# Kernel optimization log

Hardware: AMD Instinct MI355X
Metric: run time of the kernel (lower is better)

The kernel has to match this reference:

```python
import jax, jax.numpy as jnp
import numpy as np
import math

D = 128
SAMPLE_RATE = 16000
F_MIN = 40.0
WINDOW_SAMPLES = 400
DECAY_C = 4.0
B, L = 8, 80000


def _mel_freqs(num, f_min, f_max):
    m_min = 2595.0 * np.log10(1.0 + f_min / 700.0)
    m_max = 2595.0 * np.log10(1.0 + f_max / 700.0)
    mels = np.linspace(m_min, m_max, num)
    return 700.0 * (10.0 ** (mels / 2595.0) - 1.0)


def setup_inputs() -> dict:
    key = jax.random.key(0)
    k_x, k_phase = jax.random.split(key)
    x = jax.random.normal(k_x, (B, L), dtype=jnp.float32)

    freqs_hz = _mel_freqs(D, F_MIN, SAMPLE_RATE / 2)
    omega = jnp.asarray(2.0 * math.pi * freqs_hz / SAMPLE_RATE, dtype=jnp.float32)

    alpha_mag = DECAY_C / WINDOW_SAMPLES  # 0.01
    alpha_raw = jnp.full((D,), math.log(math.expm1(alpha_mag)), dtype=jnp.float32)
    b_log_mag = jnp.full((D,), math.log(math.sqrt(2.0 * alpha_mag)), dtype=jnp.float32)
    b_phase = 2.0 * math.pi * jax.random.uniform(k_phase, (D,), dtype=jnp.float32)

    # K = ceil(log(1/1e-5)/alpha_mag) rounded up to 64, clipped to [64, L] -> 1152
    K = int(math.ceil(math.log(1.0 / 1e-5) / alpha_mag))
    K = max(64, min(K, L))
    K = (K + 63) // 64 * 64
    K = min(K, L)

    return {"x": x, "omega": omega, "alpha_raw": alpha_raw,
            "b_log_mag": b_log_mag, "b_phase": b_phase, "K": K}


def reference(x, omega, alpha_raw, b_log_mag, b_phase, K):
    # Analytic Gabor taps: g(tau) = |b| * exp(alpha*tau) * exp(i*(phi + omega*tau))
    alpha = -jax.nn.softplus(alpha_raw)            # (D,), alpha < 0
    b_mag = jnp.exp(b_log_mag)                     # (D,)
    tau = jnp.arange(K, dtype=x.dtype)             # (K,)
    envelope = jnp.exp(alpha[None, :] * tau[:, None])          # (K, D)
    phase = b_phase[None, :] + omega[None, :] * tau[:, None]   # (K, D)
    scale = b_mag[None, :] * envelope
    g_real = scale * jnp.cos(phase)                # (K, D)
    g_imag = scale * jnp.sin(phase)                # (K, D)

    # Causal correlation with flipped taps -> causal FIR convolution.
    # weight: (2D, 1, K) = [real filters; imag filters]
    g_real_f = jnp.flip(g_real, axis=0).T          # (D, K)
    g_imag_f = jnp.flip(g_imag, axis=0).T          # (D, K)
    weight = jnp.concatenate([g_real_f, g_imag_f], axis=0)[:, None, :]  # (2D,1,K)

    x_padded = jnp.pad(x[:, None, :], ((0, 0), (0, 0), (K - 1, 0)))  # (B,1,L+K-1)
    H = jax.lax.conv_general_dilated(
        x_padded, weight, window_strides=(1,), padding='VALID',
        dimension_numbers=('NCW', 'OIW', 'NCW'))   # (B, 2D, L)

    H_real, H_imag = H[:, :D, :], H[:, D:, :]
    power = H_real * H_real + H_imag * H_imag      # |H|^2, return_power=True path
    return jnp.transpose(power, (0, 2, 1))         # (B, L, D)
```

## Files before the change

### kernel.cpp

```cpp
#include <hip/hip_runtime.h>
#include <math.h>


#define BB 8
#define LL 80000
#define DD 128
#define CHUNK 500
#define NCHUNK 160
#define KMAX 1152

#define STEP(xv)                                   \
    {                                              \
        float t1 = fmaf(-ei, si, (xv));            \
        float nr = fmaf(er, sr, t1);               \
        float ni = fmaf(er, si, ei * sr);          \
        sr = nr; si = ni;                          \
    }

__global__ __launch_bounds__(DD) void sstfr_kernel(
    const float* __restrict__ x,
    const float* __restrict__ omega,
    const float* __restrict__ alpha_raw,
    const float* __restrict__ b_log_mag,
    const int*   __restrict__ Kp,
    float*       __restrict__ out)
{
    __shared__ __align__(16) float xs[KMAX + CHUNK];

    const int d     = threadIdx.x;
    const int chunk = blockIdx.x;
    const int b     = blockIdx.y;

    int K = Kp[0];
    K = (K + 3) & ~3;
    if (K > KMAX) K = KMAX;

    const int t0    = chunk * CHUNK;
    const int base  = t0 - K;
    const int total = CHUNK + K;
    const float* xb = x + (size_t)b * LL;

    for (int i = d; i < total; i += DD) {
        const int idx = base + i;
        xs[i] = (idx >= 0 && idx < LL) ? xb[idx] : 0.0f;
    }
    __syncthreads();

    const float w     = omega[d];
    const float alpha = -log1pf(expf(alpha_raw[d]));
    const float ea    = expf(alpha);
    const float er    = ea * cosf(w);
    const float ei    = ea * sinf(w);
    const float scale = expf(2.0f * b_log_mag[d]);

    float sr = 0.0f, si = 0.0f;

    const float4* x4 = (const float4*)xs;
    const int g0 = K >> 2;
    const int gT = total >> 2;

    float4 cur = x4[0];

    for (int q = 0; q < g0; ++q) {
        float4 nxt = x4[q + 1];
        STEP(cur.x) STEP(cur.y) STEP(cur.z) STEP(cur.w)
        cur = nxt;
    }

    float* op = out + ((size_t)b * LL + t0) * DD + d;
    for (int q = g0; q < gT - 1; ++q) {
        float4 nxt = x4[q + 1];
        STEP(cur.x) op[0 * DD] = scale * fmaf(sr, sr, si * si);
        STEP(cur.y) op[1 * DD] = scale * fmaf(sr, sr, si * si);
        STEP(cur.z) op[2 * DD] = scale * fmaf(sr, sr, si * si);
        STEP(cur.w) op[3 * DD] = scale * fmaf(sr, sr, si * si);
        op += 4 * DD;
        cur = nxt;
    }
    STEP(cur.x) op[0 * DD] = scale * fmaf(sr, sr, si * si);
    STEP(cur.y) op[1 * DD] = scale * fmaf(sr, sr, si * si);
    STEP(cur.z) op[2 * DD] = scale * fmaf(sr, sr, si * si);
    STEP(cur.w) op[3 * DD] = scale * fmaf(sr, sr, si * si);
}

extern "C" void kernel_launch(void* const* d_in, const int* in_sizes, int n_in,
                              void* d_out, int out_size, void* d_ws, size_t ws_size,
                              hipStream_t stream) {
    const float* x         = (const float*)d_in[0];
    const float* omega     = (const float*)d_in[1];
    const float* alpha_raw = (const float*)d_in[2];
    const float* b_log_mag = (const float*)d_in[3];
    const int*   Kp        = (const int*)d_in[5];
    float* out = (float*)d_out;

    dim3 grid(NCHUNK, BB);
    dim3 block(DD);
    sstfr_kernel<<<grid, block, 0, stream>>>(x, omega, alpha_raw, b_log_mag, Kp, out);
}
```

Measured before the change: 357.3 us.

## Split chunks into two sub-blocks and stage output through LDS for vector stores

Each block now runs 256 threads, two groups of 128 channels, each handling a 200-sample sub-chunk of a 400-sample chunk. Each group runs its own K-sample warmup of the recurrence. Per-step power values go into a double-buffered LDS tile and are written out as contiguous 16-byte nontemporal vector stores instead of scalar strided stores. This aims to improve store coalescing and raise parallelism, at the cost of more redundant warmup work and a __syncthreads per 4-sample group.

```diff
diff --git a/kernel.cpp b/kernel.cpp
--- a/kernel.cpp
+++ b/kernel.cpp
@@ -5,9 +5,14 @@
 #define BB 8
 #define LL 80000
 #define DD 128
-#define CHUNK 500
-#define NCHUNK 160
+#define CHUNK 400
+#define SUB 200
+#define NCHUNK 200
 #define KMAX 1152
+#define NT 256
+#define GMAIN (SUB / 4)
+
+typedef __attribute__((ext_vector_type(4))) float f4;
 
 #define STEP(xv)                                   \
     {                                              \
@@ -17,7 +22,22 @@
         sr = nr; si = ni;                          \
     }
 
-__global__ __launch_bounds__(DD) void sstfr_kernel(
+#define GROUP_BODY(qq)                                                   \
+    {                                                                    \
+        float p0, p1, p2, p3;                                            \
+        STEP(cur.x) p0 = scale * fmaf(sr, sr, si * si);                  \
+        STEP(cur.y) p1 = scale * fmaf(sr, sr, si * si);                  \
+        STEP(cur.z) p2 = scale * fmaf(sr, sr, si * si);                  \
+        STEP(cur.w) p3 = scale * fmaf(sr, sr, si * si);                  \
+        float* tw = &tb[(qq) & 1][sub * 512 + d];                        \
+        tw[0] = p0; tw[128] = p1; tw[256] = p2; tw[384] = p3;            \
+        __syncthreads();                                                 \
+        const f4 v = *(const f4*)&tb[(qq) & 1][4 * tid];                 \
+        __builtin_nontemporal_store(v, op4 + slot);                      \
+        op4 += 128;                                                      \
+    }
+
+__global__ __launch_bounds__(NT) void sstfr_kernel(
     const float* __restrict__ x,
     const float* __restrict__ omega,
     const float* __restrict__ alpha_raw,
@@ -26,8 +46,11 @@
     float*       __restrict__ out)
 {
     __shared__ __align__(16) float xs[KMAX + CHUNK];
+    __shared__ __align__(16) float tb[2][4 * NT];
 
-    const int d     = threadIdx.x;
+    const int tid  = threadIdx.x;
+    const int d    = tid & (DD - 1);
+    const int sub  = tid >> 7;
     const int chunk = blockIdx.x;
     const int b     = blockIdx.y;
 
@@ -40,7 +63,7 @@
     const int total = CHUNK + K;
     const float* xb = x + (size_t)b * LL;
 
-    for (int i = d; i < total; i += DD) {
+    for (int i = tid; i < total; i += NT) {
         const int idx = base + i;
         xs[i] = (idx >= 0 && idx < LL) ? xb[idx] : 0.0f;
     }
@@ -55,9 +78,8 @@
 
     float sr = 0.0f, si = 0.0f;
 
-    const float4* x4 = (const float4*)xs;
+    const float4* x4 = (const float4*)xs + sub * (SUB / 4);
     const int g0 = K >> 2;
-    const int gT = total >> 2;
 
     float4 cur = x4[0];
 
@@ -67,20 +89,15 @@
         cur = nxt;
     }
 
-    float* op = out + ((size_t)b * LL + t0) * DD + d;
-    for (int q = g0; q < gT - 1; ++q) {
-        float4 nxt = x4[q + 1];
-        STEP(cur.x) op[0 * DD] = scale * fmaf(sr, sr, si * si);
-        STEP(cur.y) op[1 * DD] = scale * fmaf(sr, sr, si * si);
-        STEP(cur.z) op[2 * DD] = scale * fmaf(sr, sr, si * si);
-        STEP(cur.w) op[3 * DD] = scale * fmaf(sr, sr, si * si);
-        op += 4 * DD;
+    f4* op4 = (f4*)(out + ((size_t)b * LL + t0 + sub * SUB) * DD);
+    const int slot = tid & 127;
+
+    for (int q = 0; q < GMAIN - 1; ++q) {
+        float4 nxt = x4[g0 + q + 1];
+        GROUP_BODY(q)
         cur = nxt;
     }
-    STEP(cur.x) op[0 * DD] = scale * fmaf(sr, sr, si * si);
-    STEP(cur.y) op[1 * DD] = scale * fmaf(sr, sr, si * si);
-    STEP(cur.z) op[2 * DD] = scale * fmaf(sr, sr, si * si);
-    STEP(cur.w) op[3 * DD] = scale * fmaf(sr, sr, si * si);
+    GROUP_BODY(GMAIN - 1)
 }
 
 extern "C" void kernel_launch(void* const* d_in, const int* in_sizes, int n_in,
@@ -94,6 +111,6 @@
     float* out = (float*)d_out;
 
     dim3 grid(NCHUNK, BB);
-    dim3 block(DD);
+    dim3 block(NT);
     sstfr_kernel<<<grid, block, 0, stream>>>(x, omega, alpha_raw, b_log_mag, Kp, out);
 }
```

Measured after the change: 350.3 us. Within noise of the previous version (-1.9%).

## Split recurrence into warm-up state kernel and streaming output kernel

Applied to the files above, without the earlier changes.

Splits the per-chunk IIR recurrence into two launches. The first kernel runs the K-sample warm-up for each chunk and stores the complex state in workspace. The second kernel starts from that state and emits only the chunk's outputs. Chunk size also drops from 500 to 400, giving more blocks. The aim is to move the long warm-up off the store-heavy streaming path and to raise parallelism, at the cost of an extra launch and a small workspace round trip.

```diff
diff --git a/kernel.cpp b/kernel.cpp
--- a/kernel.cpp
+++ b/kernel.cpp
@@ -5,9 +5,10 @@
 #define BB 8
 #define LL 80000
 #define DD 128
-#define CHUNK 500
-#define NCHUNK 160
+#define CHUNK 400
+#define NCHUNK 200
 #define KMAX 1152
+#define NT 128
 
 #define STEP(xv)                                   \
     {                                              \
@@ -17,33 +18,73 @@
         sr = nr; si = ni;                          \
     }
 
-__global__ __launch_bounds__(DD) void sstfr_kernel(
+__global__ __launch_bounds__(NT) void sstfr_state(
     const float* __restrict__ x,
     const float* __restrict__ omega,
     const float* __restrict__ alpha_raw,
-    const float* __restrict__ b_log_mag,
     const int*   __restrict__ Kp,
-    float*       __restrict__ out)
+    float2*      __restrict__ ws)
 {
-    __shared__ __align__(16) float xs[KMAX + CHUNK];
+    __shared__ __align__(16) float xs[KMAX];
 
-    const int d     = threadIdx.x;
-    const int chunk = blockIdx.x;
-    const int b     = blockIdx.y;
+    const int d = threadIdx.x;
+    const int c = blockIdx.x;
+    const int b = blockIdx.y;
 
     int K = Kp[0];
     K = (K + 3) & ~3;
     if (K > KMAX) K = KMAX;
 
-    const int t0    = chunk * CHUNK;
-    const int base  = t0 - K;
-    const int total = CHUNK + K;
+    const int base = c * CHUNK - K;
     const float* xb = x + (size_t)b * LL;
 
-    for (int i = d; i < total; i += DD) {
+    for (int i = d; i < K; i += NT) {
         const int idx = base + i;
-        xs[i] = (idx >= 0 && idx < LL) ? xb[idx] : 0.0f;
+        xs[i] = (idx >= 0) ? xb[idx] : 0.0f;
     }
+    __syncthreads();
+
+    const float w     = omega[d];
+    const float alpha = -log1pf(expf(alpha_raw[d]));
+    const float ea    = expf(alpha);
+    const float er    = ea * cosf(w);
+    const float ei    = ea * sinf(w);
+
+    float sr = 0.0f, si = 0.0f;
+
+    const float4* x4 = (const float4*)xs;
+    const int g0 = K >> 2;
+
+    float4 cur = x4[0];
+    for (int q = 0; q < g0 - 1; ++q) {
+        float4 nxt = x4[q + 1];
+        STEP(cur.x) STEP(cur.y) STEP(cur.z) STEP(cur.w)
+        cur = nxt;
+    }
+    STEP(cur.x) STEP(cur.y) STEP(cur.z) STEP(cur.w)
+
+    ws[((size_t)b * NCHUNK + c) * DD + d] = make_float2(sr, si);
+}
+
+__global__ __launch_bounds__(NT) void sstfr_stream(
+    const float* __restrict__ x,
+    const float* __restrict__ omega,
+    const float* __restrict__ alpha_raw,
+    const float* __restrict__ b_log_mag,
+    const float2* __restrict__ ws,
+    float*       __restrict__ out)
+{
+    __shared__ __align__(16) float xs[CHUNK];
+
+    const int d = threadIdx.x;
+    const int c = blockIdx.x;
+    const int b = blockIdx.y;
+
+    const int t0 = c * CHUNK;
+    const float* xb = x + (size_t)b * LL + t0;
+
+    for (int i = d; i < CHUNK; i += NT)
+        xs[i] = xb[i];
     __syncthreads();
 
     const float w     = omega[d];
@@ -53,22 +94,16 @@
     const float ei    = ea * sinf(w);
     const float scale = expf(2.0f * b_log_mag[d]);
 
-    float sr = 0.0f, si = 0.0f;
+    const float2 s0 = ws[((size_t)b * NCHUNK + c) * DD + d];
+    float sr = s0.x, si = s0.y;
+
+    float* op = out + ((size_t)b * LL + t0) * DD + d;
 
     const float4* x4 = (const float4*)xs;
-    const int g0 = K >> 2;
-    const int gT = total >> 2;
+    const int gT = CHUNK >> 2;
 
     float4 cur = x4[0];
-
-    for (int q = 0; q < g0; ++q) {
-        float4 nxt = x4[q + 1];
-        STEP(cur.x) STEP(cur.y) STEP(cur.z) STEP(cur.w)
-        cur = nxt;
-    }
-
-    float* op = out + ((size_t)b * LL + t0) * DD + d;
-    for (int q = g0; q < gT - 1; ++q) {
+    for (int q = 0; q < gT - 1; ++q) {
         float4 nxt = x4[q + 1];
         STEP(cur.x) op[0 * DD] = scale * fmaf(sr, sr, si * si);
         STEP(cur.y) op[1 * DD] = scale * fmaf(sr, sr, si * si);
@@ -91,9 +126,11 @@
     const float* alpha_raw = (const float*)d_in[2];
     const float* b_log_mag = (const float*)d_in[3];
     const int*   Kp        = (const int*)d_in[5];
-    float* out = (float*)d_out;
+    float*  out = (float*)d_out;
+    float2* ws  = (float2*)d_ws;
 
     dim3 grid(NCHUNK, BB);
-    dim3 block(DD);
-    sstfr_kernel<<<grid, block, 0, stream>>>(x, omega, alpha_raw, b_log_mag, Kp, out);
+    dim3 block(NT);
+    sstfr_state<<<grid, block, 0, stream>>>(x, omega, alpha_raw, Kp, ws);
+    sstfr_stream<<<grid, block, 0, stream>>>(x, omega, alpha_raw, b_log_mag, ws, out);
 }
```

Measured after the change: 374.4 us. +4.8%, slower.
